# Kernel optimization log

Hardware: AMD Instinct MI355X
Metric: run time of the kernel (lower is better)

## Reference

```python
import jax, jax.numpy as jnp
import numpy as np

D_MODEL = 1024
LN_EPS = 1e-5


def setup_inputs() -> dict:
    key = jax.random.key(0)
    ks = jax.random.split(key, 12)
    d = D_MODEL
    std_qkv = np.sqrt(2.0 / (d + d / 16)).astype(np.float32)
    std_fc = np.sqrt(2.0 / (d + d)).astype(np.float32)  # xavier_normal for square matrix
    inp = {
        "x": jax.random.normal(ks[0], (2, 2048, d), dtype=jnp.float32),
        "Wq": jax.random.normal(ks[1], (d, d), dtype=jnp.float32) * std_qkv,
        "bq": jnp.zeros((d,), dtype=jnp.float32),
        "Wk": jax.random.normal(ks[2], (d, d), dtype=jnp.float32) * std_qkv,
        "bk": jnp.zeros((d,), dtype=jnp.float32),
        "Wv": jax.random.normal(ks[3], (d, d), dtype=jnp.float32) * std_qkv,
        "bv": jnp.zeros((d,), dtype=jnp.float32),
        "Wfc": jax.random.normal(ks[4], (d, d), dtype=jnp.float32) * std_fc,
        "bfc": jnp.zeros((d,), dtype=jnp.float32),
        "gamma": jnp.ones((d,), dtype=jnp.float32),
        "beta": jnp.zeros((d,), dtype=jnp.float32),
        "n_heads": 16,
    }
    return inp


def reference(x, Wq, bq, Wk, bk, Wv, bv, Wfc, bfc, gamma, beta, n_heads):
    b, l, d = x.shape
    dk = d // n_heads

    def proj2(t, W, bias):
        # Faithful to original: projection applied TWICE (w_qs(w_qs(input)) etc.)
        t = t @ W.T + bias
        return t @ W.T + bias

    def split_heads(t):
        # b l (h dk) -> h b l dk
        return t.reshape(b, l, n_heads, dk).transpose(2, 0, 1, 3)

    q = split_heads(proj2(x, Wq, bq))
    k = split_heads(proj2(x, Wk, bk))
    v = split_heads(proj2(x, Wv, bv))

    scores = jnp.einsum("hblk,hbtk->hblt", q, k) / np.sqrt(dk).astype(np.float32)
    attn = jax.nn.softmax(scores, axis=3)
    out = jnp.einsum("hblt,hbtv->hblv", attn, v)
    out = out.transpose(1, 2, 0, 3).reshape(b, l, d)  # h b l v -> b l (h v)
    out = out @ Wfc.T + bfc  # dropout = identity in eval
    out = out + x

    mu = jnp.mean(out, axis=-1, keepdims=True)
    var = jnp.mean(jnp.square(out - mu), axis=-1, keepdims=True)
    out = (out - mu) * jax.lax.rsqrt(var + LN_EPS) * gamma + beta
    return (out, attn)
```

## Files before the change

### kernel.cpp

```cpp
#include <hip/hip_runtime.h>
#include <hip/hip_bf16.h>

typedef unsigned short u16;
typedef float  f32x4  __attribute__((ext_vector_type(4)));
typedef short  bf16x8 __attribute__((ext_vector_type(8)));
typedef u16    u16x4  __attribute__((ext_vector_type(4)));
typedef u16    u16x8  __attribute__((ext_vector_type(8)));

__device__ __forceinline__ u16 f2bf(float f) {
    union { __hip_bfloat16 b; u16 u; } c;
    c.b = __float2bfloat16(f);
    return c.u;
}
__device__ __forceinline__ float bf2f(u16 u) {
    union { unsigned i; float f; } c;
    c.i = ((unsigned)u) << 16;
    return c.f;
}

__device__ __forceinline__ void gl2lds16(const u16* g, u16* l) {
    __builtin_amdgcn_global_load_lds(
        (const __attribute__((address_space(1))) void*)g,
        (__attribute__((address_space(3))) void*)l,
        16, 0, 0);
}

__global__ __launch_bounds__(256) void prep(const float* __restrict__ x,
                                            const float* __restrict__ Wq,
                                            const float* __restrict__ bq,
                                            const float* __restrict__ Wk,
                                            const float* __restrict__ bk,
                                            const float* __restrict__ Wv,
                                            const float* __restrict__ bv,
                                            const float* __restrict__ Wfc,
                                            u16* __restrict__ Xb,
                                            u16* __restrict__ Wallb,
                                            u16* __restrict__ Wfcb,
                                            u16* __restrict__ Wallt,
                                            float* __restrict__ ball2) {
    const int b = blockIdx.x, tid = threadIdx.x;
    __shared__ u16 t[64][72];
    if (b < 4096) {
        int i = b * 256 + tid;
        float4 v = ((const float4*)x)[i];
        u16x4 o = { f2bf(v.x), f2bf(v.y), f2bf(v.z), f2bf(v.w) };
        ((u16x4*)Xb)[i] = o;
    } else if (b < 8192) {
        int i = b - 4096;
        int z = i >> 10, blk = i & 1023;
        const float* src = z == 0 ? Wq : z == 1 ? Wk : z == 2 ? Wv : Wfc;
        u16* dst = z < 3 ? Wallb + (size_t)z * 1048576 : Wfcb;
        int j = blk * 256 + tid;
        float4 v = ((const float4*)src)[j];
        u16x4 o = { f2bf(v.x), f2bf(v.y), f2bf(v.z), f2bf(v.w) };
        ((u16x4*)dst)[j] = o;
    } else if (b < 8960) {
        int i = b - 8192;
        int z = i >> 8, rem = i & 255;
        const float* src = z == 0 ? Wq : z == 1 ? Wk : Wv;
        u16* dst = Wallt + (size_t)z * 1048576;
        const int tr = (rem >> 4) * 64, tc = (rem & 15) * 64;
        const int r4 = tid >> 4;
        const int c4 = (tid & 15) * 4;
#pragma unroll
        for (int rr = 0; rr < 4; ++rr) {
            int r = rr * 16 + r4;
            float4 v = *(const float4*)&src[(size_t)(tr + r) * 1024 + tc + c4];
            t[r][c4] = f2bf(v.x); t[r][c4 + 1] = f2bf(v.y);
            t[r][c4 + 2] = f2bf(v.z); t[r][c4 + 3] = f2bf(v.w);
        }
        __syncthreads();
#pragma unroll
        for (int rr = 0; rr < 4; ++rr) {
            int oc = rr * 16 + r4;
            u16x4 o = { t[c4][oc], t[c4 + 1][oc], t[c4 + 2][oc], t[c4 + 3][oc] };
            *(u16x4*)&dst[(size_t)(tc + oc) * 1024 + tr + c4] = o;
        }
    } else {
        int i = b - 8960;
        int z = i >> 8, bx = i & 255;
        const float* W = z == 0 ? Wq : z == 1 ? Wk : Wv;
        const float* bias = z == 0 ? bq : z == 1 ? bk : bv;
        const int row  = bx * 4 + (tid >> 6);
        const int lane = tid & 63;
        float4 w  = ((const float4*)(W + (size_t)row * 1024))[lane];
        float4 bb = ((const float4*)bias)[lane];
        float s = w.x * bb.x + w.y * bb.y + w.z * bb.z + w.w * bb.w;
#pragma unroll
        for (int d = 1; d < 64; d <<= 1) s += __shfl_xor(s, d);
        if (lane == 0) ball2[z * 1024 + row] = s + bias[row];
    }
}

__global__ __launch_bounds__(256) void transV(const u16* __restrict__ QKV,
                                              u16* __restrict__ VT) {
    const int kt = blockIdx.x, bb = blockIdx.y, h = blockIdx.z;
    __shared__ u16 t[64][72];
    const int tid = threadIdx.x;
    {
        const int key = tid >> 3, d8 = (tid & 7) * 8;
        const u16* src = QKV + 2048 +
            ((size_t)(bb * 2048 + kt * 64 + key)) * 3072 + h * 64 + d8;
        *(u16x8*)&t[key][d8]      = *(const u16x8*)src;
        *(u16x8*)&t[key + 32][d8] = *(const u16x8*)(src + (size_t)32 * 3072);
    }
    __syncthreads();
    {
        const int dk = tid >> 3, k8 = (tid & 7) * 8;
        u16* dst = VT + ((size_t)((bb * 16 + h) * 64 + dk)) * 2048 + kt * 64 + k8;
        u16x8 o0, o1;
#pragma unroll
        for (int j = 0; j < 8; ++j) { o0[j] = t[k8 + j][dk]; o1[j] = t[k8 + j][dk + 32]; }
        *(u16x8*)dst = o0;
        *(u16x8*)(dst + (size_t)32 * 2048) = o1;
    }
}

template<int OUTF32>
__global__ __launch_bounds__(256) void gemm_bt(const u16* __restrict__ A,
                                               const u16* __restrict__ B,
                                               const float* __restrict__ bias,
                                               void* __restrict__ Cout,
                                               int M, int N, int K,
                                               size_t zA, size_t zB, size_t zC,
                                               const float* __restrict__ xres) {
    __shared__ __align__(16) u16 As[128 * 32];
    __shared__ __align__(16) u16 Bs[128 * 32];

    const int tid  = threadIdx.x;
    const int lane = tid & 63;
    const int w    = tid >> 6;
    const int lr   = lane & 15;
    const int lg   = lane >> 4;
    const int wr   = (w >> 1) * 64;
    const int wc   = (w & 1) * 64;
    const int bm   = blockIdx.x * 128;
    const int bn   = blockIdx.y * 128;
    const int z    = blockIdx.z;
    A += (size_t)z * zA;
    B += (size_t)z * zB;
    char* Cz = (char*)Cout + (size_t)z * zC * (OUTF32 ? 4 : 2);

    const int srow = w * 32 + (lane >> 2);
    const int scol = (lane & 3) * 8;
    u16* la = &As[(w * 32) * 32];
    u16* lb = &Bs[(w * 32) * 32];

    f32x4 acc[4][4] = {};

    for (int k0 = 0; k0 < K; k0 += 32) {
        const u16* Ag = A + (size_t)(bm + srow) * K + k0 + scol;
        const u16* Bg = B + (size_t)(bn + srow) * K + k0 + scol;
        gl2lds16(Ag, la);
        gl2lds16(Ag + (size_t)16 * K, la + 16 * 32);
        gl2lds16(Bg, lb);
        gl2lds16(Bg + (size_t)16 * K, lb + 16 * 32);
        __syncthreads();

        bf16x8 af[4], bfr[4];
#pragma unroll
        for (int i = 0; i < 4; ++i)
            af[i] = *(const bf16x8*)&As[(wr + i * 16 + lr) * 32 + lg * 8];
#pragma unroll
        for (int j = 0; j < 4; ++j)
            bfr[j] = *(const bf16x8*)&Bs[(wc + j * 16 + lr) * 32 + lg * 8];
#pragma unroll
        for (int i = 0; i < 4; ++i)
#pragma unroll
            for (int j = 0; j < 4; ++j)
                acc[i][j] = __builtin_amdgcn_mfma_f32_16x16x32_bf16(
                    af[i], bfr[j], acc[i][j], 0, 0, 0);
        __syncthreads();
    }

#pragma unroll
    for (int i = 0; i < 4; ++i) {
        const int grow = bm + wr + i * 16 + lg * 4;
#pragma unroll
        for (int j = 0; j < 4; ++j) {
            const int gcol = bn + wc + j * 16 + lr;
            const float bv = bias ? bias[gcol] : 0.f;
#pragma unroll
            for (int r = 0; r < 4; ++r) {
                float v = acc[i][j][r] + bv;
                if (OUTF32) {
                    if (xres) v += xres[(size_t)(grow + r) * N + gcol];
                    ((float*)Cz)[(size_t)(grow + r) * N + gcol] = v;
                } else {
                    ((u16*)Cz)[(size_t)(grow + r) * N + gcol] = f2bf(v);
                }
            }
        }
    }
}

__global__ __launch_bounds__(256, 4) void lsumK(const u16* __restrict__ QKV,
                                                float* __restrict__ rl_g) {
    const int hw  = blockIdx.x;
    const int L   = (hw & 7) * 64 + (hw >> 3);
    const int qb  = L & 15;
    const int bbh = L >> 4;
    const int bb  = bbh >> 4;
    const int h   = bbh & 15;
    const int tid = threadIdx.x, lane = tid & 63, w = tid >> 6;
    const int lr = lane & 15, lg = lane >> 4;

    __shared__ __align__(16) u16 smem[12288];

    const int qrow0 = qb * 128 + w * 32;
    bf16x8 qf[2][2];
#pragma unroll
    for (int qg = 0; qg < 2; ++qg) {
        const size_t qoff =
            ((size_t)bb * 2048 + qrow0 + qg * 16 + lr) * 3072 + h * 64 + lg * 8;
        qf[qg][0] = *(const bf16x8*)&QKV[qoff];
        qf[qg][1] = *(const bf16x8*)&QKV[qoff + 32];
    }

    const int srow  = lane >> 3;
    const int sslot = (lane & 7) ^ srow;
    const u16* kg0 = QKV + 1024 + ((size_t)bb * 2048 + w * 16 + srow) * 3072 + h * 64 + sslot * 8;

    const int swz   = (lr & 7) << 3;
    const int offk0 = (lg * 8) ^ swz;
    const int offk1 = (32 + lg * 8) ^ swz;
    const int rowB  = lr * 64;
    const float SC  = 0.18033688011112042f;

    auto stageKto = [&](int kt, int ldsOff) {
        const u16* s = kg0 + (size_t)kt * 64 * 3072;
        gl2lds16(s,                    smem + ldsOff + (w * 16) * 64);
        gl2lds16(s + (size_t)8 * 3072, smem + ldsOff + (w * 16 + 8) * 64);
    };

    float lsum[2][4] = {};
    stageKto(0, 0);
    stageKto(1, 4096);
    for (int kt = 0; kt < 32; ++kt) {
        if (kt < 31) asm volatile("s_waitcnt vmcnt(2)" ::: "memory");
        else         asm volatile("s_waitcnt vmcnt(0)" ::: "memory");
        __builtin_amdgcn_s_barrier();
        const u16* Kb = smem + (kt % 3) * 4096;
        __builtin_amdgcn_s_setprio(1);
#pragma unroll
        for (int jb = 0; jb < 4; ++jb) {
            bf16x8 kf0 = *(const bf16x8*)&Kb[jb * 1024 + rowB + offk0];
            bf16x8 kf1 = *(const bf16x8*)&Kb[jb * 1024 + rowB + offk1];
#pragma unroll
            for (int qg = 0; qg < 2; ++qg) {
                f32x4 acc = {0.f, 0.f, 0.f, 0.f};
                acc = __builtin_amdgcn_mfma_f32_16x16x32_bf16(qf[qg][0], kf0, acc, 0, 0, 0);
                acc = __builtin_amdgcn_mfma_f32_16x16x32_bf16(qf[qg][1], kf1, acc, 0, 0, 0);
#pragma unroll
                for (int r = 0; r < 4; ++r)
                    lsum[qg][r] += __builtin_amdgcn_exp2f(acc[r] * SC);
            }
        }
        __builtin_amdgcn_s_setprio(0);
        if (kt < 30) stageKto(kt + 2, ((kt + 2) % 3) * 4096);
    }
#pragma unroll
    for (int qg = 0; qg < 2; ++qg)
#pragma unroll
        for (int r = 0; r < 4; ++r) {
#pragma unroll
            for (int d = 1; d < 16; d <<= 1)
                lsum[qg][r] += __shfl_xor(lsum[qg][r], d);
        }
    if (lr == 0) {
        const size_t base = (size_t)(h * 2 + bb) * 2048 + qrow0;
#pragma unroll
        for (int qg = 0; qg < 2; ++qg)
#pragma unroll
            for (int r = 0; r < 4; ++r)
                rl_g[base + qg * 16 + lg * 4 + r] = 1.f / lsum[qg][r];
    }
}

__global__ __launch_bounds__(256, 4) void attnPO(const u16* __restrict__ QKV,
                                                 const u16* __restrict__ VT,
                                                 const float* __restrict__ rl_g,
                                                 float* __restrict__ P,
                                                 u16* __restrict__ O) {
    const int hw  = blockIdx.x;
    const int L   = (hw & 7) * 128 + (hw >> 3);
    const int qb  = L & 31;
    const int bbh = L >> 5;
    const int bb  = bbh >> 4;
    const int h   = bbh & 15;
    const int tid = threadIdx.x, lane = tid & 63, w = tid >> 6;
    const int lr = lane & 15, lg = lane >> 4;

    __shared__ __align__(16) u16 smem[20480];

    const int qrow0 = qb * 64 + w * 16;
    const size_t qoff = ((size_t)bb * 2048 + qrow0 + lr) * 3072 + h * 64 + lg * 8;
    const bf16x8 qf0 = *(const bf16x8*)&QKV[qoff];
    const bf16x8 qf1 = *(const bf16x8*)&QKV[qoff + 32];

    const size_t prowb = (size_t)(h * 2 + bb) * 2048 + qrow0;
    float rl[4];
#pragma unroll
    for (int r = 0; r < 4; ++r) rl[r] = rl_g[prowb + lg * 4 + r];

    const int srow  = lane >> 3;
    const int sslot = (lane & 7) ^ srow;
    const u16* kg0 = QKV + 1024 + ((size_t)bb * 2048 + w * 16 + srow) * 3072 + h * 64 + sslot * 8;
    const u16* vg0 = VT + ((size_t)((bb * 16 + h) * 64) + w * 16 + srow) * 2048 + sslot * 8;

    const int swz   = (lr & 7) << 3;
    const int offk0 = (lg * 8) ^ swz;
    const int offk1 = (32 + lg * 8) ^ swz;
    const int rowB  = lr * 64;
    const float SC  = 0.18033688011112042f;

    auto stageKto = [&](int kt, int ldsOff) {
        const u16* s = kg0 + (size_t)kt * 64 * 3072;
        gl2lds16(s,                    smem + ldsOff + (w * 16) * 64);
        gl2lds16(s + (size_t)8 * 3072, smem + ldsOff + (w * 16 + 8) * 64);
    };
    auto stageVto = [&](int kt, int ldsOff) {
        const u16* s = vg0 + kt * 64;
        gl2lds16(s,                    smem + ldsOff + (w * 16) * 64);
        gl2lds16(s + (size_t)8 * 2048, smem + ldsOff + (w * 16 + 8) * 64);
    };

    f32x4 oacc[4] = {};
    const int wrow = lane >> 4;
    const int wcol = (lane & 15) * 4;
    u16* Psw = smem + 16384 + w * 1024;

    stageKto(0, 0); stageVto(0, 8192);
    for (int kt = 0; kt < 32; ++kt) {
        const int cur = kt & 1;
        if (kt == 0) {
            stageKto(1, 4096); stageVto(1, 12288);
            asm volatile("s_waitcnt vmcnt(4)" ::: "memory");
        } else if (kt < 31) {
            stageKto(kt + 1, (cur ^ 1) * 4096);
            stageVto(kt + 1, 8192 + (cur ^ 1) * 4096);
            asm volatile("s_waitcnt vmcnt(8)" ::: "memory");
        } else {
            asm volatile("s_waitcnt vmcnt(4)" ::: "memory");
        }
        __builtin_amdgcn_s_barrier();

        const u16* Kb = smem + cur * 4096;
        const u16* Vb = smem + 8192 + cur * 4096;

        __builtin_amdgcn_s_setprio(1);
#pragma unroll
        for (int jb = 0; jb < 4; ++jb) {
            bf16x8 kf0 = *(const bf16x8*)&Kb[jb * 1024 + rowB + offk0];
            bf16x8 kf1 = *(const bf16x8*)&Kb[jb * 1024 + rowB + offk1];
            f32x4 acc = {0.f, 0.f, 0.f, 0.f};
            acc = __builtin_amdgcn_mfma_f32_16x16x32_bf16(qf0, kf0, acc, 0, 0, 0);
            acc = __builtin_amdgcn_mfma_f32_16x16x32_bf16(qf1, kf1, acc, 0, 0, 0);
#pragma unroll
            for (int r = 0; r < 4; ++r) {
                float p = __builtin_amdgcn_exp2f(acc[r] * SC) * rl[r];
                const int row = lg * 4 + r;
                Psw[row * 64 + ((jb * 16 + lr) ^ ((row & 7) << 3))] = f2bf(p);
            }
        }
        __builtin_amdgcn_s_setprio(0);
#pragma unroll
        for (int rr = 0; rr < 4; ++rr) {
            const int row = rr * 4 + wrow;
            const int s = wcol >> 3, e = wcol & 7;
            u16x4 pb = *(const u16x4*)&Psw[row * 64 + ((s ^ (row & 7)) * 8) + e];
            f32x4 pv = { bf2f(pb[0]), bf2f(pb[1]), bf2f(pb[2]), bf2f(pb[3]) };
            __builtin_nontemporal_store(pv,
                (f32x4*)&P[(prowb + row) * 2048 + kt * 64 + wcol]);
        }
        __builtin_amdgcn_s_setprio(1);
#pragma unroll
        for (int kk = 0; kk < 2; ++kk) {
            const int offk = kk ? offk1 : offk0;
            bf16x8 pa = *(const bf16x8*)&Psw[rowB + offk];
#pragma unroll
            for (int dkb = 0; dkb < 4; ++dkb) {
                bf16x8 vb = *(const bf16x8*)&Vb[dkb * 1024 + rowB + offk];
                oacc[dkb] = __builtin_amdgcn_mfma_f32_16x16x32_bf16(pa, vb, oacc[dkb], 0, 0, 0);
            }
        }
        __builtin_amdgcn_s_setprio(0);
        __builtin_amdgcn_s_barrier();
    }

#pragma unroll
    for (int dkb = 0; dkb < 4; ++dkb)
#pragma unroll
        for (int r = 0; r < 4; ++r)
            O[((size_t)bb * 2048 + qrow0 + lg * 4 + r) * 1024 + h * 64 + dkb * 16 + lr] =
                f2bf(oacc[dkb][r]);
}

__global__ __launch_bounds__(256) void ln_only(float* __restrict__ Y,
                                               const float* __restrict__ gamma,
                                               const float* __restrict__ beta) {
    const int row = blockIdx.x, tid = threadIdx.x;
    const int lane = tid & 63, w = tid >> 6;
    float4 y = ((const float4*)(Y + (size_t)row * 1024))[tid];
    float t0 = y.x, t1 = y.y, t2 = y.z, t3 = y.w;
    float s  = t0 + t1 + t2 + t3;
    float ss = t0 * t0 + t1 * t1 + t2 * t2 + t3 * t3;
#pragma unroll
    for (int d = 1; d < 64; d <<= 1) { s += __shfl_xor(s, d); ss += __shfl_xor(ss, d); }
    __shared__ float as_[4], aq_[4];
    if (lane == 0) { as_[w] = s; aq_[w] = ss; }
    __syncthreads();
    s  = as_[0] + as_[1] + as_[2] + as_[3];
    ss = aq_[0] + aq_[1] + aq_[2] + aq_[3];
    const float mu  = s * (1.f / 1024.f);
    const float var = ss * (1.f / 1024.f) - mu * mu;
    const float rs  = rsqrtf(var + 1e-5f);
    float4 g  = ((const float4*)gamma)[tid];
    float4 be = ((const float4*)beta)[tid];
    float4 o;
    o.x = (t0 - mu) * rs * g.x + be.x;
    o.y = (t1 - mu) * rs * g.y + be.y;
    o.z = (t2 - mu) * rs * g.z + be.z;
    o.w = (t3 - mu) * rs * g.w + be.w;
    ((float4*)(Y + (size_t)row * 1024))[tid] = o;
}

extern "C" void kernel_launch(void* const* d_in, const int* in_sizes, int n_in,
                              void* d_out, int out_size, void* d_ws, size_t ws_size,
                              hipStream_t stream) {
    const float* x     = (const float*)d_in[0];
    const float* Wq    = (const float*)d_in[1];
    const float* bq    = (const float*)d_in[2];
    const float* Wk    = (const float*)d_in[3];
    const float* bk    = (const float*)d_in[4];
    const float* Wv    = (const float*)d_in[5];
    const float* bv    = (const float*)d_in[6];
    const float* Wfc   = (const float*)d_in[7];
    const float* bfc   = (const float*)d_in[8];
    const float* gamma = (const float*)d_in[9];
    const float* beta  = (const float*)d_in[10];

    float* out  = (float*)d_out;
    float* attn = out + (size_t)4194304;

    u16*   VT   = (u16*)d_out;
    float* rl_g = (float*)((char*)d_out + (size_t)9 * 1048576);

    char* ws = (char*)d_ws;
    u16* QKV  = (u16*)(ws);
    u16* Ob   = (u16*)(ws + (size_t)24 * 1048576);
    u16* Wfcb = (u16*)(ws + (size_t)32 * 1048576);

    char* sc = (char*)attn;
    u16*   Xb    = (u16*)sc;
    u16*   Wallb = (u16*)(sc + (size_t)8  * 1048576);
    u16*   Wallt = (u16*)(sc + (size_t)14 * 1048576);
    u16*   Wall2 = (u16*)(sc + (size_t)20 * 1048576);
    float* ball2 = (float*)(sc + (size_t)26 * 1048576);

    const size_t WSZ = 1048576;

    prep<<<9728, 256, 0, stream>>>(x, Wq, bq, Wk, bk, Wv, bv, Wfc,
                                   Xb, Wallb, Wfcb, Wallt, ball2);

    const dim3 blk(256);
    gemm_bt<0><<<dim3(8, 8, 3), blk, 0, stream>>>(Wallb, Wallt, nullptr, Wall2,
                                                  1024, 1024, 1024, WSZ, WSZ, WSZ, nullptr);
    gemm_bt<0><<<dim3(32, 24), blk, 0, stream>>>(Xb, Wall2, ball2, QKV,
                                                 4096, 3072, 1024, 0, 0, 0, nullptr);

    lsumK<<<512, 256, 0, stream>>>(QKV, rl_g);
    transV<<<dim3(32, 2, 16), 256, 0, stream>>>(QKV, VT);
    attnPO<<<1024, 256, 0, stream>>>(QKV, VT, rl_g, attn, Ob);

    gemm_bt<1><<<dim3(32, 8), blk, 0, stream>>>(Ob, Wfcb, bfc, out,
                                                4096, 1024, 1024, 0, 0, 0, x);
    ln_only<<<4096, 256, 0, stream>>>(out, gamma, beta);
}
```

Before: 281.3 us.

## Fuse V transpose into row-sum kernel, shrink its tiles, and restructure attnPO pipeline

Merges the separate transV kernel into the lsum kernel as extra blocks, removing one launch and letting the two independent jobs overlap. The lsum kernel now gives each wave 16 query rows instead of 32, which doubles the grid to 1024 compute blocks for more parallelism but makes each block load K twice as often in total. In attnPO, the prefetch of the next K/V tile now issues after a single top-of-loop barrier, and the trailing barrier is dropped. This cuts one sync per iteration but leaves less time for the load to hide behind compute.

Result: faster. 274.8 us (-2.3%).

```diff
diff --git a/kernel.cpp b/kernel.cpp
--- a/kernel.cpp
+++ b/kernel.cpp
@@ -92,30 +92,6 @@
     }
 }
 
-__global__ __launch_bounds__(256) void transV(const u16* __restrict__ QKV,
-                                              u16* __restrict__ VT) {
-    const int kt = blockIdx.x, bb = blockIdx.y, h = blockIdx.z;
-    __shared__ u16 t[64][72];
-    const int tid = threadIdx.x;
-    {
-        const int key = tid >> 3, d8 = (tid & 7) * 8;
-        const u16* src = QKV + 2048 +
-            ((size_t)(bb * 2048 + kt * 64 + key)) * 3072 + h * 64 + d8;
-        *(u16x8*)&t[key][d8]      = *(const u16x8*)src;
-        *(u16x8*)&t[key + 32][d8] = *(const u16x8*)(src + (size_t)32 * 3072);
-    }
-    __syncthreads();
-    {
-        const int dk = tid >> 3, k8 = (tid & 7) * 8;
-        u16* dst = VT + ((size_t)((bb * 16 + h) * 64 + dk)) * 2048 + kt * 64 + k8;
-        u16x8 o0, o1;
-#pragma unroll
-        for (int j = 0; j < 8; ++j) { o0[j] = t[k8 + j][dk]; o1[j] = t[k8 + j][dk + 32]; }
-        *(u16x8*)dst = o0;
-        *(u16x8*)(dst + (size_t)32 * 2048) = o1;
-    }
-}
-
 template<int OUTF32>
 __global__ __launch_bounds__(256) void gemm_bt(const u16* __restrict__ A,
                                                const u16* __restrict__ B,
@@ -194,28 +170,51 @@
     }
 }
 
-__global__ __launch_bounds__(256, 4) void lsumK(const u16* __restrict__ QKV,
-                                                float* __restrict__ rl_g) {
+__global__ __launch_bounds__(256, 4) void lsumTV(const u16* __restrict__ QKV,
+                                                 float* __restrict__ rl_g,
+                                                 u16* __restrict__ VT) {
+    __shared__ __align__(16) u16 smem[12288];
+    const int tid = threadIdx.x;
+
+    if (blockIdx.x >= 1024) {
+        const int i  = blockIdx.x - 1024;
+        const int kt = i & 31, bb = (i >> 5) & 1, h = i >> 6;
+        {
+            const int key = tid >> 3, d8 = (tid & 7) * 8;
+            const u16* src = QKV + 2048 +
+                ((size_t)(bb * 2048 + kt * 64 + key)) * 3072 + h * 64 + d8;
+            *(u16x8*)&smem[key * 72 + d8]        = *(const u16x8*)src;
+            *(u16x8*)&smem[(key + 32) * 72 + d8] = *(const u16x8*)(src + (size_t)32 * 3072);
+        }
+        __syncthreads();
+        {
+            const int dk = tid >> 3, k8 = (tid & 7) * 8;
+            u16* dst = VT + ((size_t)((bb * 16 + h) * 64 + dk)) * 2048 + kt * 64 + k8;
+            u16x8 o0, o1;
+#pragma unroll
+            for (int j = 0; j < 8; ++j) {
+                o0[j] = smem[(k8 + j) * 72 + dk];
+                o1[j] = smem[(k8 + j) * 72 + dk + 32];
+            }
+            *(u16x8*)dst = o0;
+            *(u16x8*)(dst + (size_t)32 * 2048) = o1;
+        }
+        return;
+    }
+
     const int hw  = blockIdx.x;
-    const int L   = (hw & 7) * 64 + (hw >> 3);
-    const int qb  = L & 15;
-    const int bbh = L >> 4;
+    const int L   = (hw & 7) * 128 + (hw >> 3);
+    const int qb  = L & 31;
+    const int bbh = L >> 5;
     const int bb  = bbh >> 4;
     const int h   = bbh & 15;
-    const int tid = threadIdx.x, lane = tid & 63, w = tid >> 6;
+    const int lane = tid & 63, w = tid >> 6;
     const int lr = lane & 15, lg = lane >> 4;
 
-    __shared__ __align__(16) u16 smem[12288];
-
-    const int qrow0 = qb * 128 + w * 32;
-    bf16x8 qf[2][2];
-#pragma unroll
-    for (int qg = 0; qg < 2; ++qg) {
-        const size_t qoff =
-            ((size_t)bb * 2048 + qrow0 + qg * 16 + lr) * 3072 + h * 64 + lg * 8;
-        qf[qg][0] = *(const bf16x8*)&QKV[qoff];
-        qf[qg][1] = *(const bf16x8*)&QKV[qoff + 32];
-    }
+    const int qrow0 = qb * 64 + w * 16;
+    const size_t qoff = ((size_t)bb * 2048 + qrow0 + lr) * 3072 + h * 64 + lg * 8;
+    const bf16x8 qf0 = *(const bf16x8*)&QKV[qoff];
+    const bf16x8 qf1 = *(const bf16x8*)&QKV[qoff + 32];
 
     const int srow  = lane >> 3;
     const int sslot = (lane & 7) ^ srow;
@@ -233,7 +232,7 @@
         gl2lds16(s + (size_t)8 * 3072, smem + ldsOff + (w * 16 + 8) * 64);
     };
 
-    float lsum[2][4] = {};
+    float lsum[4] = {0.f, 0.f, 0.f, 0.f};
     stageKto(0, 0);
     stageKto(1, 4096);
     for (int kt = 0; kt < 32; ++kt) {
@@ -246,34 +245,26 @@
         for (int jb = 0; jb < 4; ++jb) {
             bf16x8 kf0 = *(const bf16x8*)&Kb[jb * 1024 + rowB + offk0];
             bf16x8 kf1 = *(const bf16x8*)&Kb[jb * 1024 + rowB + offk1];
-#pragma unroll
-            for (int qg = 0; qg < 2; ++qg) {
-                f32x4 acc = {0.f, 0.f, 0.f, 0.f};
-                acc = __builtin_amdgcn_mfma_f32_16x16x32_bf16(qf[qg][0], kf0, acc, 0, 0, 0);
-                acc = __builtin_amdgcn_mfma_f32_16x16x32_bf16(qf[qg][1], kf1, acc, 0, 0, 0);
-#pragma unroll
-                for (int r = 0; r < 4; ++r)
-                    lsum[qg][r] += __builtin_amdgcn_exp2f(acc[r] * SC);
-            }
+            f32x4 acc = {0.f, 0.f, 0.f, 0.f};
+            acc = __builtin_amdgcn_mfma_f32_16x16x32_bf16(qf0, kf0, acc, 0, 0, 0);
+            acc = __builtin_amdgcn_mfma_f32_16x16x32_bf16(qf1, kf1, acc, 0, 0, 0);
+#pragma unroll
+            for (int r = 0; r < 4; ++r)
+                lsum[r] += __builtin_amdgcn_exp2f(acc[r] * SC);
         }
         __builtin_amdgcn_s_setprio(0);
         if (kt < 30) stageKto(kt + 2, ((kt + 2) % 3) * 4096);
     }
 #pragma unroll
-    for (int qg = 0; qg < 2; ++qg)
-#pragma unroll
-        for (int r = 0; r < 4; ++r) {
-#pragma unroll
-            for (int d = 1; d < 16; d <<= 1)
-                lsum[qg][r] += __shfl_xor(lsum[qg][r], d);
-        }
+    for (int r = 0; r < 4; ++r) {
+#pragma unroll
+        for (int d = 1; d < 16; d <<= 1) lsum[r] += __shfl_xor(lsum[r], d);
+    }
     if (lr == 0) {
         const size_t base = (size_t)(h * 2 + bb) * 2048 + qrow0;
 #pragma unroll
-        for (int qg = 0; qg < 2; ++qg)
-#pragma unroll
-            for (int r = 0; r < 4; ++r)
-                rl_g[base + qg * 16 + lg * 4 + r] = 1.f / lsum[qg][r];
+        for (int r = 0; r < 4; ++r)
+            rl_g[base + lg * 4 + r] = 1.f / lsum[r];
     }
 }
 
@@ -333,17 +324,13 @@
     stageKto(0, 0); stageVto(0, 8192);
     for (int kt = 0; kt < 32; ++kt) {
         const int cur = kt & 1;
-        if (kt == 0) {
-            stageKto(1, 4096); stageVto(1, 12288);
-            asm volatile("s_waitcnt vmcnt(4)" ::: "memory");
-        } else if (kt < 31) {
+        if (kt == 0) asm volatile("s_waitcnt vmcnt(0)" ::: "memory");
+        else         asm volatile("s_waitcnt vmcnt(4)" ::: "memory");
+        __builtin_amdgcn_s_barrier();
+        if (kt < 31) {
             stageKto(kt + 1, (cur ^ 1) * 4096);
             stageVto(kt + 1, 8192 + (cur ^ 1) * 4096);
-            asm volatile("s_waitcnt vmcnt(8)" ::: "memory");
-        } else {
-            asm volatile("s_waitcnt vmcnt(4)" ::: "memory");
-        }
-        __builtin_amdgcn_s_barrier();
+        }
 
         const u16* Kb = smem + cur * 4096;
         const u16* Vb = smem + 8192 + cur * 4096;
@@ -385,7 +372,6 @@
             }
         }
         __builtin_amdgcn_s_setprio(0);
-        __builtin_amdgcn_s_barrier();
     }
 
 #pragma unroll
@@ -469,8 +455,7 @@
     gemm_bt<0><<<dim3(32, 24), blk, 0, stream>>>(Xb, Wall2, ball2, QKV,
                                                  4096, 3072, 1024, 0, 0, 0, nullptr);
 
-    lsumK<<<512, 256, 0, stream>>>(QKV, rl_g);
-    transV<<<dim3(32, 2, 16), 256, 0, stream>>>(QKV, VT);
+    lsumTV<<<2048, 256, 0, stream>>>(QKV, rl_g, VT);
     attnPO<<<1024, 256, 0, stream>>>(QKV, VT, rl_g, attn, Ob);
 
     gemm_bt<1><<<dim3(32, 8), blk, 0, stream>>>(Ob, Wfcb, bfc, out,
```
